# Performance work log

Hardware: AMD Instinct MI355X
Metric: run time of the kernel (lower is better)

## Reference

```python
import jax, jax.numpy as jnp
import numpy as np

NUM_EXPERT = 8
TOP_K = 2
DIM = 1024
EPS = 1e-8

def setup_inputs() -> dict:
    key = jax.random.key(0)
    ks = jax.random.split(key, 8)
    B, S, D, E, F = 2, 2048, DIM, NUM_EXPERT, 4 * DIM
    scale = 0.02
    return {
        "x": jax.random.normal(ks[0], (B, S, D), jnp.float32),
        "noise": jax.random.normal(ks[1], (B, S, E), jnp.float32),
        "gate_w": jax.random.normal(ks[2], (D, E), jnp.float32) * scale,
        "gate_b": jnp.zeros((E,), jnp.float32),
        "noise_w": jax.random.normal(ks[3], (D, E), jnp.float32) * scale,
        "noise_b": jnp.zeros((E,), jnp.float32),
        "w1": jax.random.normal(ks[4], (E, D, F), jnp.float32) * scale,
        "b1": jnp.zeros((E, F), jnp.float32),
        "w2": jax.random.normal(ks[5], (E, F, D), jnp.float32) * scale,
        "b2": jnp.zeros((E, D), jnp.float32),
    }


def reference(x, noise, gate_w, gate_b, noise_w, noise_b, w1, b1, w2, b2):
    B, S, D = x.shape
    E = gate_w.shape[-1]
    # --- router (noise passed in explicitly instead of randn_like) ---
    logits = (x @ gate_w + gate_b) + noise + (x @ noise_w + noise_b)  # [B,S,E]
    top_val, top_ids = jax.lax.top_k(logits, TOP_K)                   # [B,S,K]
    # mask of selected experts; scores = softmax over top-k logits, 0 elsewhere
    sel = jax.nn.one_hot(top_ids, E, dtype=jnp.bool_).any(axis=-2)    # [B,S,E]
    neg_inf = jnp.asarray(-jnp.inf, logits.dtype)
    scores = jax.nn.softmax(jnp.where(sel, logits, neg_inf), axis=-1)  # [B,S,E]

    flat_x = x.reshape(-1, D)            # [T,D]
    flat_s = scores.reshape(-1, E)       # [T,E]
    # dense per-expert FFN; non-selected experts have exactly-zero weight,
    # so the weighted combine matches the masked gather/scatter loop.
    h = jax.nn.silu(jnp.einsum('td,edf->etf', flat_x, w1) + b1[:, None, :])  # [E,T,F]
    eo = jnp.einsum('etf,efd->etd', h, w2) + b2[:, None, :]                  # [E,T,D]
    out = jnp.einsum('te,etd->td', flat_s, eo).reshape(B, S, D)

    # --- aux load-balancing loss: KL(uniform || importance), reduction=sum ---
    importance = flat_s.mean(axis=0)                  # [E]
    u = jnp.full_like(importance, 1.0 / E)
    aux_loss = jnp.sum(u * (jnp.log(u) - jnp.log(importance + EPS)))
    return out, aux_loss
```

## Files before the change

### kernel.cpp

```cpp
#include <hip/hip_runtime.h>
#include <hip/hip_bf16.h>
#include <cstdint>
#include <cstddef>

#define T_TOK 4096
#define D_DIM 1024
#define E_NUM 8
#define F_DIM 4096

typedef __bf16 bf16_t;
typedef bf16_t bf16x8 __attribute__((ext_vector_type(8)));
typedef float f32x4 __attribute__((ext_vector_type(4)));

__device__ __forceinline__ void gl_lds16(const void* g, void* l) {
    __builtin_amdgcn_global_load_lds(
        (const __attribute__((address_space(1))) unsigned int*)g,
        (__attribute__((address_space(3))) unsigned int*)l,
        16, 0, 0);
}

#define F_W1T    0ull
#define F_W2T    67108864ull
#define F_HT     134217728ull
#define F_XBF    209715200ull
#define F_ROWV   218103808ull
#define F_SCORES 251658240ull
#define F_TOK    (F_SCORES + 131072ull)
#define F_SC     (F_TOK    + 131072ull)
#define F_T2R    (F_SC     + 131072ull)
#define F_CNT    (F_T2R    + 32768ull)
#define F_OFF    (F_CNT    + 32ull)
#define F_BLK    (F_OFF    + 32ull)
#define FAST_NEED (F_BLK + 32ull)

#define WS_H      0ull
#define WS_ROWV   (WS_H      + 8192ull*4096*2)
#define WS_SCORES (WS_ROWV   + 8192ull*1024*4)
#define WS_TOK    (WS_SCORES + 4096ull*8*4)
#define WS_SC     (WS_TOK    + 8ull*4096*4)
#define WS_T2R    (WS_SC     + 8ull*4096*4)
#define WS_CNT    (WS_T2R    + 4096ull*2*4)
#define WS_OFF    (WS_CNT    + 32ull)
#define WS_BLK    (WS_OFF    + 32ull)

__global__ __launch_bounds__(256) void router_k(
    const float* __restrict__ x, const float* __restrict__ noise,
    const float* __restrict__ gate_w, const float* __restrict__ gate_b,
    const float* __restrict__ noise_w, const float* __restrict__ noise_b,
    float* __restrict__ scores, int* __restrict__ tok_tmp,
    float* __restrict__ sc_tmp, int* __restrict__ tok2row, int* __restrict__ counts)
{
    int t = blockIdx.x * 4 + (threadIdx.x >> 6);
    int lane = threadIdx.x & 63;
    const float* xr = x + (size_t)t * D_DIM;
    float acc[8] = {0,0,0,0,0,0,0,0};
    for (int d = lane; d < D_DIM; d += 64) {
        float xv = xr[d];
#pragma unroll
        for (int e = 0; e < 8; e++)
            acc[e] += xv * (gate_w[d*8+e] + noise_w[d*8+e]);
    }
#pragma unroll
    for (int e = 0; e < 8; e++) {
#pragma unroll
        for (int m = 1; m < 64; m <<= 1)
            acc[e] += __shfl_xor(acc[e], m);
    }
    float lg[8];
#pragma unroll
    for (int e = 0; e < 8; e++)
        lg[e] = acc[e] + gate_b[e] + noise_b[e] + noise[t*8+e];
    int e1 = 0; float v1 = lg[0];
#pragma unroll
    for (int e = 1; e < 8; e++) if (lg[e] > v1) { v1 = lg[e]; e1 = e; }
    int e2 = -1; float v2 = -INFINITY;
#pragma unroll
    for (int e = 0; e < 8; e++) if (e != e1 && lg[e] > v2) { v2 = lg[e]; e2 = e; }
    float ex = expf(v2 - v1);
    float den = 1.0f + ex;
    float s1 = 1.0f / den, s2 = ex / den;
    if (lane < 8)
        scores[t*8+lane] = (lane==e1) ? s1 : ((lane==e2) ? s2 : 0.0f);
    if (lane == 0) {
        int p1 = atomicAdd(&counts[e1], 1);
        tok_tmp[e1*T_TOK + p1] = t; sc_tmp[e1*T_TOK + p1] = s1;
        tok2row[t*2]   = (e1<<16) | p1;
        int p2 = atomicAdd(&counts[e2], 1);
        tok_tmp[e2*T_TOK + p2] = t; sc_tmp[e2*T_TOK + p2] = s2;
        tok2row[t*2+1] = (e2<<16) | p2;
    }
}

__global__ void prefix_k(const int* __restrict__ counts, int* __restrict__ offsets,
                         int* __restrict__ blk_off) {
    if (threadIdx.x == 0) {
        int o = 0, b = 0;
        for (int e = 0; e < 8; e++) {
            offsets[e] = o; blk_off[e] = b;
            o += counts[e]; b += (counts[e] + 127) >> 7;
        }
    }
}

__global__ __launch_bounds__(256) void aux_k(const float* __restrict__ scores,
                                             float* __restrict__ out_aux) {
    __shared__ float part[256];
    int i = threadIdx.x;
    int e = i & 7, g = i >> 3;
    float s = 0.f;
    for (int t = g; t < T_TOK; t += 32) s += scores[t*8+e];
    part[i] = s; __syncthreads();
    for (int st = 128; st >= 8; st >>= 1) {
        if (i < st) part[i] += part[i+st];
        __syncthreads();
    }
    if (i == 0) {
        float aux = 0.f;
        for (int ee = 0; ee < 8; ee++) {
            float imp = part[ee] * (1.0f / (float)T_TOK);
            aux += 0.125f * (logf(0.125f) - logf(imp + 1e-8f));
        }
        *out_aux = aux;
    }
}

__global__ __launch_bounds__(256) void prep_w_k(
    const float* __restrict__ src, bf16_t* __restrict__ dst,
    int ksb, int ntb, int Kdim, int Ndim)
{
    size_t cid = (size_t)blockIdx.x * 256 + threadIdx.x;
    int kc = cid & 3;
    int n  = (cid >> 2) & 127;
    int ks = (cid >> 9) & ((1 << ksb) - 1);
    int nt = (cid >> (9 + ksb)) & ((1 << ntb) - 1);
    int e  = (int)(cid >> (9 + ksb + ntb));
    int kcd = kc ^ ((n >> 1) & 3);
    int k0 = ks * 32 + kcd * 8;
    const float* s = src + ((size_t)e * Kdim + k0) * Ndim + nt * 128 + n;
    union { bf16_t u[8]; bf16x8 v; } pk;
#pragma unroll
    for (int j = 0; j < 8; j++) pk.u[j] = (bf16_t)s[(size_t)j * Ndim];
    *(bf16x8*)(dst + cid * 8) = pk.v;
}

__global__ __launch_bounds__(256) void prep_x_k(const float* __restrict__ x,
                                                bf16_t* __restrict__ xb) {
    size_t i = ((size_t)blockIdx.x * 256 + threadIdx.x) * 8;
    f32x4 a = *(const f32x4*)(x + i);
    f32x4 b = *(const f32x4*)(x + i + 4);
    union { bf16_t u[8]; bf16x8 v; } pk;
#pragma unroll
    for (int j = 0; j < 4; j++) { pk.u[j] = (bf16_t)a[j]; pk.u[4+j] = (bf16_t)b[j]; }
    *(bf16x8*)(xb + i) = pk.v;
}

__global__ __launch_bounds__(256) void ffn1_fast_k(
    const bf16_t* __restrict__ xb, const bf16_t* __restrict__ w1t,
    const float* __restrict__ b1, const int* __restrict__ tok_tmp,
    const int* __restrict__ counts, const int* __restrict__ blk_off,
    char* __restrict__ h_t)
{
    int bx = blockIdx.x;
    int nt = bx & 31, mt = (bx >> 5) & 31, e = bx >> 10;
    int ne = counts[e];
    if (mt * 128 >= ne) return;

    __shared__ alignas(16) char smem[16384];
    int tid = threadIdx.x, w = tid >> 6, l = tid & 63;

    int srow0 = w * 32 + (l >> 2);
    int kcd = (l & 3) ^ ((l >> 3) & 3);
    int g0r = mt * 128 + srow0, g1r = g0r + 16;
    int tok0 = tok_tmp[e * T_TOK + (g0r < ne ? g0r : 0)];
    int tok1 = tok_tmp[e * T_TOK + (g1r < ne ? g1r : 0)];
    const char* gA0 = (const char*)(xb + (size_t)tok0 * D_DIM + kcd * 8);
    const char* gA1 = (const char*)(xb + (size_t)tok1 * D_DIM + kcd * 8);
    const char* gB0 = (const char*)w1t + ((size_t)(e * 32 + nt) * 32) * 8192
                      + w * 2048 + l * 16;
    const char* gB1 = gB0 + 1024;
    char* lA0 = smem + w * 2048;
    char* lA1 = lA0 + 1024;
    char* lB0 = smem + 8192 + w * 2048;
    char* lB1 = lB0 + 1024;

    int fr = l & 15, kq = l >> 4;
    int csel = (kq ^ ((fr >> 1) & 3)) << 4;
    int wm = (w & 1) * 64, wn = (w >> 1) * 64;
    int aoff[4], boff[4];
#pragma unroll
    for (int i = 0; i < 4; i++) {
        aoff[i] = (wm + i * 16 + fr) * 64 + csel;
        boff[i] = 8192 + (wn + i * 16 + fr) * 64 + csel;
    }

    f32x4 acc[4][4] = {};
    for (int ks = 0; ks < 32; ks++) {
        gl_lds16(gA0, lA0); gl_lds16(gA1, lA1);
        gl_lds16(gB0, lB0); gl_lds16(gB1, lB1);
        gA0 += 64; gA1 += 64; gB0 += 8192; gB1 += 8192;
        __syncthreads();
        bf16x8 af[4], bf[4];
#pragma unroll
        for (int i = 0; i < 4; i++) af[i] = *(const bf16x8*)(smem + aoff[i]);
#pragma unroll
        for (int i = 0; i < 4; i++) bf[i] = *(const bf16x8*)(smem + boff[i]);
#pragma unroll
        for (int mi = 0; mi < 4; mi++)
#pragma unroll
            for (int ni = 0; ni < 4; ni++)
                acc[mi][ni] = __builtin_amdgcn_mfma_f32_16x16x32_bf16(af[mi], bf[ni], acc[mi][ni], 0, 0, 0);
        __syncthreads();
    }

    int quad = l >> 4;
    size_t htBase = (size_t)(blk_off[e] + mt) * 1048576ull;
    const float* b1e = b1 + (size_t)e * F_DIM + nt * 128;
    for (int rnd = 0; rnd < 4; rnd++) {
        if ((w >> 1) == (rnd >> 1)) {
            int nb0 = (rnd & 1) * 2;
#pragma unroll
            for (int nn = 0; nn < 2; nn++) {
                int cl = nn * 16 + fr;
                float bb = b1e[rnd * 32 + cl];
#pragma unroll
                for (int mi = 0; mi < 4; mi++) {
                    int rbase = wm + mi * 16 + quad * 4;
#pragma unroll
                    for (int r = 0; r < 4; r++) {
                        int row = rbase + r;
                        float v = acc[mi][nb0 + nn][r] + bb;
                        v = v / (1.0f + expf(-v));
                        int off = row * 64 + (((cl >> 3) ^ ((row >> 1) & 3)) << 4) + ((cl & 7) << 1);
                        *(bf16_t*)(smem + off) = (bf16_t)v;
                    }
                }
            }
        }
        __syncthreads();
        {
            size_t sub = htBase + (size_t)(nt * 4 + rnd) * 8192;
            *(f32x4*)(h_t + sub + tid * 16)         = *(const f32x4*)(smem + tid * 16);
            *(f32x4*)(h_t + sub + (tid + 256) * 16) = *(const f32x4*)(smem + (tid + 256) * 16);
        }
        __syncthreads();
    }
}

__global__ __launch_bounds__(256) void ffn2_fast_k(
    const char* __restrict__ h_t, const bf16_t* __restrict__ w2t,
    const float* __restrict__ b2, const float* __restrict__ sc_tmp,
    const int* __restrict__ counts, const int* __restrict__ offsets,
    const int* __restrict__ blk_off, float* __restrict__ rowv)
{
    int bx = blockIdx.x;
    int nt = bx & 7, mt = (bx >> 3) & 31, e = bx >> 8;
    int ne = counts[e];
    if (mt * 128 >= ne) return;

    __shared__ alignas(16) char smem[18944];
    int tid = threadIdx.x, w = tid >> 6, l = tid & 63;
    float* rowsc = (float*)(smem + 18432);
    if (tid < 128) {
        int r = mt * 128 + tid;
        rowsc[tid] = (r < ne) ? sc_tmp[e * T_TOK + r] : 0.0f;
    }

    const char* gA0 = h_t + (size_t)(blk_off[e] + mt) * 1048576ull + w * 2048 + l * 16;
    const char* gA1 = gA0 + 1024;
    const char* gB0 = (const char*)w2t + ((size_t)(e * 8 + nt) * 128) * 8192
                      + w * 2048 + l * 16;
    const char* gB1 = gB0 + 1024;
    char* lA0 = smem + w * 2048;
    char* lA1 = lA0 + 1024;
    char* lB0 = smem + 8192 + w * 2048;
    char* lB1 = lB0 + 1024;

    int fr = l & 15, kq = l >> 4;
    int csel = (kq ^ ((fr >> 1) & 3)) << 4;
    int wm = (w & 1) * 64, wn = (w >> 1) * 64;
    int aoff[4], boff[4];
#pragma unroll
    for (int i = 0; i < 4; i++) {
        aoff[i] = (wm + i * 16 + fr) * 64 + csel;
        boff[i] = 8192 + (wn + i * 16 + fr) * 64 + csel;
    }

    f32x4 acc[4][4] = {};
    for (int ks = 0; ks < 128; ks++) {
        gl_lds16(gA0, lA0); gl_lds16(gA1, lA1);
        gl_lds16(gB0, lB0); gl_lds16(gB1, lB1);
        gA0 += 8192; gA1 += 8192; gB0 += 8192; gB1 += 8192;
        __syncthreads();
        bf16x8 af[4], bf[4];
#pragma unroll
        for (int i = 0; i < 4; i++) af[i] = *(const bf16x8*)(smem + aoff[i]);
#pragma unroll
        for (int i = 0; i < 4; i++) bf[i] = *(const bf16x8*)(smem + boff[i]);
#pragma unroll
        for (int mi = 0; mi < 4; mi++)
#pragma unroll
            for (int ni = 0; ni < 4; ni++)
                acc[mi][ni] = __builtin_amdgcn_mfma_f32_16x16x32_bf16(af[mi], bf[ni], acc[mi][ni], 0, 0, 0);
        __syncthreads();
    }

    int quad = l >> 4;
    int off_e = offsets[e];
    const float* b2e = b2 + (size_t)e * D_DIM + nt * 128;
    float* Ct = (float*)smem;
    for (int rnd = 0; rnd < 4; rnd++) {
        if ((w >> 1) == (rnd >> 1)) {
            int nb0 = (rnd & 1) * 2;
#pragma unroll
            for (int nn = 0; nn < 2; nn++) {
                int cl = nn * 16 + fr;
                float bb = b2e[rnd * 32 + cl];
#pragma unroll
                for (int mi = 0; mi < 4; mi++) {
                    int rbase = wm + mi * 16 + quad * 4;
#pragma unroll
                    for (int r = 0; r < 4; r++) {
                        int row = rbase + r;
                        Ct[row * 36 + cl] = (acc[mi][nb0 + nn][r] + bb) * rowsc[row];
                    }
                }
            }
        }
        __syncthreads();
        {
            int row = tid >> 1, h = tid & 1;
            if (mt * 128 + row < ne) {
                float* dst = rowv + (size_t)(off_e + mt * 128 + row) * D_DIM
                           + nt * 128 + rnd * 32 + h * 16;
                const float* src = Ct + row * 36 + h * 16;
#pragma unroll
                for (int j = 0; j < 4; j++)
                    *(f32x4*)(dst + j * 4) = *(const f32x4*)(src + j * 4);
            }
        }
        __syncthreads();
    }
}

__global__ __launch_bounds__(256) void combine_k(
    const float* __restrict__ rowv, const int* __restrict__ tok2row,
    const int* __restrict__ offsets, float* __restrict__ out)
{
    int t = blockIdx.x;
    int p0 = tok2row[t*2], p1 = tok2row[t*2+1];
    int r0 = offsets[p0 >> 16] + (p0 & 0xffff);
    int r1 = offsets[p1 >> 16] + (p1 & 0xffff);
    int d = threadIdx.x * 4;
    f32x4 a = *(const f32x4*)(rowv + (size_t)r0 * D_DIM + d);
    f32x4 b = *(const f32x4*)(rowv + (size_t)r1 * D_DIM + d);
    *(f32x4*)(out + (size_t)t * D_DIM + d) = a + b;
}

#define BM 128
#define BN 128
#define BK 32
#define LDA 40
#define LDCB 136
#define LDCF 68
#define SMEM_BYTES 35328

__global__ __launch_bounds__(256) void ffn1_fb_k(
    const float* __restrict__ x, const float* __restrict__ w1, const float* __restrict__ b1,
    const int* __restrict__ tok_tmp, const int* __restrict__ counts,
    const int* __restrict__ offsets, bf16_t* __restrict__ h)
{
    int e  = blockIdx.x >> 5;
    int mt = blockIdx.x & 31;
    int nt = blockIdx.y;
    int ne = counts[e];
    if (mt * BM >= ne) return;
    int nb = nt * BN;
    const float* W = w1 + (size_t)e * D_DIM * F_DIM;

    __shared__ alignas(16) char smem[SMEM_BYTES];
    bf16_t* As = (bf16_t*)smem;
    bf16_t* Bs = (bf16_t*)(smem + 10240);
    int* rowtok = (int*)(smem + 34816);

    int tid = threadIdx.x;
    if (tid < 128) {
        int r = mt*BM + tid;
        rowtok[tid] = (r < ne) ? tok_tmp[e*T_TOK + r] : -1;
    }
    __syncthreads();

    f32x4 acc[4][4] = {};
    int wave = tid >> 6, lane = tid & 63;
    int wm = (wave & 1) * 64, wn = (wave >> 1) * 64;
    int fr = lane & 15, fk = (lane >> 4) * 8;
    int sr = tid >> 1, sh = (tid & 1) * 16;
    int bn_ = tid & 127, bk_ = (tid >> 7) * 16;

    for (int k0 = 0; k0 < D_DIM; k0 += BK) {
        {
            int tok = rowtok[sr];
            union { bf16_t u[16]; bf16x8 v[2]; } pk;
            if (tok >= 0) {
                const float* src = x + (size_t)tok * D_DIM + k0 + sh;
#pragma unroll
                for (int j = 0; j < 16; j++) pk.u[j] = (bf16_t)src[j];
            } else {
#pragma unroll
                for (int j = 0; j < 16; j++) pk.u[j] = (bf16_t)0.0f;
            }
            *(bf16x8*)(As + sr*LDA + sh)     = pk.v[0];
            *(bf16x8*)(As + sr*LDA + sh + 8) = pk.v[1];
        }
        {
            union { bf16_t u[16]; bf16x8 v[2]; } pk;
            const float* src = W + (size_t)(k0 + bk_) * F_DIM + nb + bn_;
#pragma unroll
            for (int j = 0; j < 16; j++) pk.u[j] = (bf16_t)src[(size_t)j * F_DIM];
            *(bf16x8*)(Bs + bn_*LDA + bk_)     = pk.v[0];
            *(bf16x8*)(Bs + bn_*LDA + bk_ + 8) = pk.v[1];
        }
        __syncthreads();
        bf16x8 af[4], bfr[4];
#pragma unroll
        for (int i = 0; i < 4; i++) af[i]  = *(bf16x8*)(As + (wm + i*16 + fr)*LDA + fk);
#pragma unroll
        for (int i = 0; i < 4; i++) bfr[i] = *(bf16x8*)(Bs + (wn + i*16 + fr)*LDA + fk);
#pragma unroll
        for (int mi = 0; mi < 4; mi++)
#pragma unroll
            for (int ni = 0; ni < 4; ni++)
                acc[mi][ni] = __builtin_amdgcn_mfma_f32_16x16x32_bf16(af[mi], bfr[ni], acc[mi][ni], 0, 0, 0);
        __syncthreads();
    }

    bf16_t* Ct = (bf16_t*)smem;
    const float* b1e = b1 + (size_t)e * F_DIM + nb;
#pragma unroll
    for (int mi = 0; mi < 4; mi++) {
        int row = wm + mi*16 + ((lane >> 4) << 2);
#pragma unroll
        for (int ni = 0; ni < 4; ni++) {
            int col = wn + ni*16 + fr;
            float bb = b1e[col];
#pragma unroll
            for (int r = 0; r < 4; r++) {
                float v = acc[mi][ni][r] + bb;
                float sv = v / (1.0f + expf(-v));
                Ct[(row + r)*LDCB + col] = (bf16_t)sv;
            }
        }
    }
    __syncthreads();
    {
        int row = tid >> 1, seg = (tid & 1) * 64;
        if (mt*BM + row < ne) {
            int grow = offsets[e] + mt*BM + row;
            bf16_t* dst = h + (size_t)grow * F_DIM + nb + seg;
#pragma unroll
            for (int j = 0; j < 8; j++)
                *(bf16x8*)(dst + j*8) = *(bf16x8*)(Ct + row*LDCB + seg + j*8);
        }
    }
}

__global__ __launch_bounds__(256) void ffn2_fb_k(
    const bf16_t* __restrict__ h, const float* __restrict__ w2, const float* __restrict__ b2,
    const float* __restrict__ sc_tmp, const int* __restrict__ counts,
    const int* __restrict__ offsets, float* __restrict__ rowv)
{
    int e  = blockIdx.x >> 5;
    int mt = blockIdx.x & 31;
    int nt = blockIdx.y;
    int ne = counts[e];
    if (mt * BM >= ne) return;
    int nb = nt * BN;
    int off = offsets[e];
    const float* W = w2 + (size_t)e * F_DIM * D_DIM;

    __shared__ alignas(16) char smem[SMEM_BYTES];
    bf16_t* As = (bf16_t*)smem;
    bf16_t* Bs = (bf16_t*)(smem + 10240);
    float* rowsc = (float*)(smem + 34816);

    int tid = threadIdx.x;
    if (tid < 128) {
        int r = mt*BM + tid;
        rowsc[tid] = (r < ne) ? sc_tmp[e*T_TOK + r] : 0.0f;
    }
    __syncthreads();

    f32x4 acc[4][4] = {};
    int wave = tid >> 6, lane = tid & 63;
    int wm = (wave & 1) * 64, wnn = wave >> 1;
    int fr = lane & 15, fk = (lane >> 4) * 8;
    int sr = tid >> 1, sh = (tid & 1) * 16;
    int bn_ = tid & 127, bk_ = (tid >> 7) * 16;
    bool arow_valid = (mt*BM + sr) < ne;
    const bf16_t* asrc0 = h + (size_t)(off + mt*BM + sr) * F_DIM + sh;

    for (int k0 = 0; k0 < F_DIM; k0 += BK) {
        {
            bf16x8 v0, v1;
            if (arow_valid) {
                v0 = *(const bf16x8*)(asrc0 + k0);
                v1 = *(const bf16x8*)(asrc0 + k0 + 8);
            } else {
                v0 = (bf16x8)(bf16_t)0.0f; v1 = (bf16x8)(bf16_t)0.0f;
            }
            *(bf16x8*)(As + sr*LDA + sh)     = v0;
            *(bf16x8*)(As + sr*LDA + sh + 8) = v1;
        }
        {
            union { bf16_t u[16]; bf16x8 v[2]; } pk;
            const float* src = W + (size_t)(k0 + bk_) * D_DIM + nb + bn_;
#pragma unroll
            for (int j = 0; j < 16; j++) pk.u[j] = (bf16_t)src[(size_t)j * D_DIM];
            *(bf16x8*)(Bs + bn_*LDA + bk_)     = pk.v[0];
            *(bf16x8*)(Bs + bn_*LDA + bk_ + 8) = pk.v[1];
        }
        __syncthreads();
        bf16x8 af[4], bfr[4];
#pragma unroll
        for (int i = 0; i < 4; i++) af[i]  = *(bf16x8*)(As + (wm + i*16 + fr)*LDA + fk);
#pragma unroll
        for (int i = 0; i < 4; i++) bfr[i] = *(bf16x8*)(Bs + (wnn*64 + i*16 + fr)*LDA + fk);
#pragma unroll
        for (int mi = 0; mi < 4; mi++)
#pragma unroll
            for (int ni = 0; ni < 4; ni++)
                acc[mi][ni] = __builtin_amdgcn_mfma_f32_16x16x32_bf16(af[mi], bfr[ni], acc[mi][ni], 0, 0, 0);
        __syncthreads();
    }

    const float* b2e = b2 + (size_t)e * D_DIM + nb;
    float* Ctf = (float*)smem;
    for (int half = 0; half < 2; half++) {
        if (wnn == half) {
#pragma unroll
            for (int mi = 0; mi < 4; mi++) {
                int row = wm + mi*16 + ((lane >> 4) << 2);
#pragma unroll
                for (int ni = 0; ni < 4; ni++) {
                    int lcol = ni*16 + fr;
                    float bb = b2e[half*64 + lcol];
#pragma unroll
                    for (int r = 0; r < 4; r++) {
                        float v = (acc[mi][ni][r] + bb) * rowsc[row + r];
                        Ctf[(row + r)*LDCF + lcol] = v;
                    }
                }
            }
        }
        __syncthreads();
        {
            int row = tid >> 1, seg = (tid & 1) * 32;
            if (mt*BM + row < ne) {
                float* dst = rowv + (size_t)(off + mt*BM + row) * D_DIM + nb + half*64 + seg;
#pragma unroll
                for (int j = 0; j < 8; j++)
                    *(f32x4*)(dst + j*4) = *(f32x4*)(Ctf + row*LDCF + seg + j*4);
            }
        }
        __syncthreads();
    }
}

extern "C" void kernel_launch(void* const* d_in, const int* in_sizes, int n_in,
                              void* d_out, int out_size, void* d_ws, size_t ws_size,
                              hipStream_t stream) {
    const float* x       = (const float*)d_in[0];
    const float* noise   = (const float*)d_in[1];
    const float* gate_w  = (const float*)d_in[2];
    const float* gate_b  = (const float*)d_in[3];
    const float* noise_w = (const float*)d_in[4];
    const float* noise_b = (const float*)d_in[5];
    const float* w1      = (const float*)d_in[6];
    const float* b1      = (const float*)d_in[7];
    const float* w2      = (const float*)d_in[8];
    const float* b2      = (const float*)d_in[9];
    float* out = (float*)d_out;
    char* ws = (char*)d_ws;

    if (ws_size >= FAST_NEED) {
        bf16_t* w1t     = (bf16_t*)(ws + F_W1T);
        bf16_t* w2t     = (bf16_t*)(ws + F_W2T);
        char*   h_t     = ws + F_HT;
        bf16_t* xb      = (bf16_t*)(ws + F_XBF);
        float*  rowv    = (float*) (ws + F_ROWV);
        float*  scores  = (float*) (ws + F_SCORES);
        int*    tok_tmp = (int*)   (ws + F_TOK);
        float*  sc_tmp  = (float*) (ws + F_SC);
        int*    tok2row = (int*)   (ws + F_T2R);
        int*    counts  = (int*)   (ws + F_CNT);
        int*    offsets = (int*)   (ws + F_OFF);
        int*    blk_off = (int*)   (ws + F_BLK);

        hipMemsetAsync(ws + F_CNT, 0, 32, stream);
        router_k<<<T_TOK/4, 256, 0, stream>>>(x, noise, gate_w, gate_b, noise_w, noise_b,
                                              scores, tok_tmp, sc_tmp, tok2row, counts);
        prefix_k<<<1, 64, 0, stream>>>(counts, offsets, blk_off);
        aux_k<<<1, 256, 0, stream>>>(scores, out + (size_t)T_TOK * D_DIM);
        prep_x_k<<<2048, 256, 0, stream>>>(x, xb);
        prep_w_k<<<16384, 256, 0, stream>>>(w1, w1t, 5, 5, D_DIM, F_DIM);
        prep_w_k<<<16384, 256, 0, stream>>>(w2, w2t, 7, 3, F_DIM, D_DIM);
        ffn1_fast_k<<<8192, 256, 0, stream>>>(xb, w1t, b1, tok_tmp, counts, blk_off, h_t);
        ffn2_fast_k<<<2048, 256, 0, stream>>>(h_t, w2t, b2, sc_tmp, counts, offsets, blk_off, rowv);
        combine_k<<<T_TOK, 256, 0, stream>>>(rowv, tok2row, offsets, out);
    } else {
        bf16_t* h       = (bf16_t*)(ws + WS_H);
        float*  rowv    = (float*) (ws + WS_ROWV);
        float*  scores  = (float*) (ws + WS_SCORES);
        int*    tok_tmp = (int*)   (ws + WS_TOK);
        float*  sc_tmp  = (float*) (ws + WS_SC);
        int*    tok2row = (int*)   (ws + WS_T2R);
        int*    counts  = (int*)   (ws + WS_CNT);
        int*    offsets = (int*)   (ws + WS_OFF);
        int*    blk_off = (int*)   (ws + WS_BLK);

        hipMemsetAsync(ws + WS_CNT, 0, 32, stream);
        router_k<<<T_TOK/4, 256, 0, stream>>>(x, noise, gate_w, gate_b, noise_w, noise_b,
                                              scores, tok_tmp, sc_tmp, tok2row, counts);
        prefix_k<<<1, 64, 0, stream>>>(counts, offsets, blk_off);
        aux_k<<<1, 256, 0, stream>>>(scores, out + (size_t)T_TOK * D_DIM);
        ffn1_fb_k<<<dim3(E_NUM*32, F_DIM/BN), 256, 0, stream>>>(x, w1, b1, tok_tmp, counts, offsets, h);
        ffn2_fb_k<<<dim3(E_NUM*32, D_DIM/BN), 256, 0, stream>>>(h, w2, b2, sc_tmp, counts, offsets, rowv);
        combine_k<<<T_TOK, 256, 0, stream>>>(rowv, tok2row, offsets, out);
    }
}
```

Measured before the change: 742.2 us.

## Fuse prep kernels, widen GEMM K-tiles to 64, store expert outputs as bf16

Merges the router, x conversion and both weight-transpose kernels into one launch, and the weight transpose now goes through an LDS tile so global reads are coalesced. Both FFN GEMMs double the K-step per iteration to 64, using a 32KB LDS tile with an 8-way XOR swizzle, which halves the number of barriers. The FFN1 epilogue writes the whole tile once instead of in four rounds. FFN2 writes its weighted per-row outputs as bf16, halving the traffic into the combine kernel, at some cost in precision.

```diff
diff --git a/kernel.cpp b/kernel.cpp
--- a/kernel.cpp
+++ b/kernel.cpp
@@ -10,6 +10,7 @@
 
 typedef __bf16 bf16_t;
 typedef bf16_t bf16x8 __attribute__((ext_vector_type(8)));
+typedef bf16_t bf16x4 __attribute__((ext_vector_type(4)));
 typedef float f32x4 __attribute__((ext_vector_type(4)));
 
 __device__ __forceinline__ void gl_lds16(const void* g, void* l) {
@@ -43,15 +44,14 @@
 #define WS_OFF    (WS_CNT    + 32ull)
 #define WS_BLK    (WS_OFF    + 32ull)
 
-__global__ __launch_bounds__(256) void router_k(
+__device__ __forceinline__ void router_body(
+    int t, int lane,
     const float* __restrict__ x, const float* __restrict__ noise,
     const float* __restrict__ gate_w, const float* __restrict__ gate_b,
     const float* __restrict__ noise_w, const float* __restrict__ noise_b,
     float* __restrict__ scores, int* __restrict__ tok_tmp,
     float* __restrict__ sc_tmp, int* __restrict__ tok2row, int* __restrict__ counts)
 {
-    int t = blockIdx.x * 4 + (threadIdx.x >> 6);
-    int lane = threadIdx.x & 63;
     const float* xr = x + (size_t)t * D_DIM;
     float acc[8] = {0,0,0,0,0,0,0,0};
     for (int d = lane; d < D_DIM; d += 64) {
@@ -91,13 +91,74 @@
     }
 }
 
+__global__ __launch_bounds__(256) void mega_prep_k(
+    const float* __restrict__ x, const float* __restrict__ noise,
+    const float* __restrict__ gate_w, const float* __restrict__ gate_b,
+    const float* __restrict__ noise_w, const float* __restrict__ noise_b,
+    const float* __restrict__ w1, const float* __restrict__ w2,
+    bf16_t* __restrict__ w1t, bf16_t* __restrict__ w2t, bf16_t* __restrict__ xb,
+    float* __restrict__ scores, int* __restrict__ tok_tmp,
+    float* __restrict__ sc_tmp, int* __restrict__ tok2row, int* __restrict__ counts)
+{
+    __shared__ alignas(16) float ftile[64 * 129];
+    int b = blockIdx.x, tid = threadIdx.x;
+    if (b < 8192) {
+        const float* src; bf16_t* dst; int Ndim;
+        if (b < 4096) {
+            int ks = b & 15, ntile = (b >> 4) & 31, e = b >> 9;
+            src = w1 + ((size_t)e * D_DIM + ks * 64) * F_DIM + ntile * 128;
+            Ndim = F_DIM;
+            dst = w1t + (((size_t)(e * 32 + ntile) * 16) + ks) * 8192;
+        } else {
+            int b2 = b - 4096;
+            int ks = b2 & 63, ntile = (b2 >> 6) & 7, e = b2 >> 9;
+            src = w2 + ((size_t)e * F_DIM + ks * 64) * D_DIM + ntile * 128;
+            Ndim = D_DIM;
+            dst = w2t + (((size_t)(e * 8 + ntile) * 64) + ks) * 8192;
+        }
+        int c0 = (tid & 31) * 4, r0 = tid >> 5;
+#pragma unroll
+        for (int i = 0; i < 8; i++) {
+            int r = r0 + i * 8;
+            f32x4 v = *(const f32x4*)(src + (size_t)r * Ndim + c0);
+#pragma unroll
+            for (int j = 0; j < 4; j++)
+                ftile[r * 129 + c0 + j] = v[j];
+        }
+        __syncthreads();
+#pragma unroll
+        for (int i = 0; i < 4; i++) {
+            int q = tid + i * 256;
+            int n = q >> 3, p = q & 7;
+            int c = p ^ (n & 7);
+            union { bf16_t u[8]; bf16x8 v; } pk;
+#pragma unroll
+            for (int jj = 0; jj < 8; jj++)
+                pk.u[jj] = (bf16_t)ftile[(c * 8 + jj) * 129 + n];
+            *(bf16x8*)(dst + (size_t)q * 8) = pk.v;
+        }
+    } else if (b < 10240) {
+        size_t i = ((size_t)(b - 8192) * 256 + tid) * 8;
+        f32x4 a = *(const f32x4*)(x + i);
+        f32x4 c = *(const f32x4*)(x + i + 4);
+        union { bf16_t u[8]; bf16x8 v; } pk;
+#pragma unroll
+        for (int j = 0; j < 4; j++) { pk.u[j] = (bf16_t)a[j]; pk.u[4+j] = (bf16_t)c[j]; }
+        *(bf16x8*)(xb + i) = pk.v;
+    } else {
+        int t = (b - 10240) * 4 + (tid >> 6);
+        router_body(t, tid & 63, x, noise, gate_w, gate_b, noise_w, noise_b,
+                    scores, tok_tmp, sc_tmp, tok2row, counts);
+    }
+}
+
 __global__ void prefix_k(const int* __restrict__ counts, int* __restrict__ offsets,
                          int* __restrict__ blk_off) {
     if (threadIdx.x == 0) {
-        int o = 0, b = 0;
+        int o = 0, bb = 0;
         for (int e = 0; e < 8; e++) {
-            offsets[e] = o; blk_off[e] = b;
-            o += counts[e]; b += (counts[e] + 127) >> 7;
+            offsets[e] = o; blk_off[e] = bb;
+            o += counts[e]; bb += (counts[e] + 127) >> 7;
         }
     }
 }
@@ -124,37 +185,7 @@
     }
 }
 
-__global__ __launch_bounds__(256) void prep_w_k(
-    const float* __restrict__ src, bf16_t* __restrict__ dst,
-    int ksb, int ntb, int Kdim, int Ndim)
-{
-    size_t cid = (size_t)blockIdx.x * 256 + threadIdx.x;
-    int kc = cid & 3;
-    int n  = (cid >> 2) & 127;
-    int ks = (cid >> 9) & ((1 << ksb) - 1);
-    int nt = (cid >> (9 + ksb)) & ((1 << ntb) - 1);
-    int e  = (int)(cid >> (9 + ksb + ntb));
-    int kcd = kc ^ ((n >> 1) & 3);
-    int k0 = ks * 32 + kcd * 8;
-    const float* s = src + ((size_t)e * Kdim + k0) * Ndim + nt * 128 + n;
-    union { bf16_t u[8]; bf16x8 v; } pk;
-#pragma unroll
-    for (int j = 0; j < 8; j++) pk.u[j] = (bf16_t)s[(size_t)j * Ndim];
-    *(bf16x8*)(dst + cid * 8) = pk.v;
-}
-
-__global__ __launch_bounds__(256) void prep_x_k(const float* __restrict__ x,
-                                                bf16_t* __restrict__ xb) {
-    size_t i = ((size_t)blockIdx.x * 256 + threadIdx.x) * 8;
-    f32x4 a = *(const f32x4*)(x + i);
-    f32x4 b = *(const f32x4*)(x + i + 4);
-    union { bf16_t u[8]; bf16x8 v; } pk;
-#pragma unroll
-    for (int j = 0; j < 4; j++) { pk.u[j] = (bf16_t)a[j]; pk.u[4+j] = (bf16_t)b[j]; }
-    *(bf16x8*)(xb + i) = pk.v;
-}
-
-__global__ __launch_bounds__(256) void ffn1_fast_k(
+__global__ __launch_bounds__(256) void ffn1_v3_k(
     const bf16_t* __restrict__ xb, const bf16_t* __restrict__ w1t,
     const float* __restrict__ b1, const int* __restrict__ tok_tmp,
     const int* __restrict__ counts, const int* __restrict__ blk_off,
@@ -165,184 +196,424 @@
     int ne = counts[e];
     if (mt * 128 >= ne) return;
 
-    __shared__ alignas(16) char smem[16384];
+    __shared__ alignas(16) char smem[32768];
     int tid = threadIdx.x, w = tid >> 6, l = tid & 63;
-
-    int srow0 = w * 32 + (l >> 2);
-    int kcd = (l & 3) ^ ((l >> 3) & 3);
-    int g0r = mt * 128 + srow0, g1r = g0r + 16;
-    int tok0 = tok_tmp[e * T_TOK + (g0r < ne ? g0r : 0)];
-    int tok1 = tok_tmp[e * T_TOK + (g1r < ne ? g1r : 0)];
-    const char* gA0 = (const char*)(xb + (size_t)tok0 * D_DIM + kcd * 8);
-    const char* gA1 = (const char*)(xb + (size_t)tok1 * D_DIM + kcd * 8);
-    const char* gB0 = (const char*)w1t + ((size_t)(e * 32 + nt) * 32) * 8192
-                      + w * 2048 + l * 16;
-    const char* gB1 = gB0 + 1024;
-    char* lA0 = smem + w * 2048;
-    char* lA1 = lA0 + 1024;
-    char* lB0 = smem + 8192 + w * 2048;
-    char* lB1 = lB0 + 1024;
+    int lc = (l & 7) ^ ((l >> 3) & 7);
+
+    const char* gA[4];
+#pragma unroll
+    for (int j = 0; j < 4; j++) {
+        int row = mt * 128 + w * 32 + j * 8 + (l >> 3);
+        int tok = tok_tmp[e * T_TOK + (row < ne ? row : 0)];
+        gA[j] = (const char*)xb + (size_t)tok * 2048 + lc * 16;
+    }
+    const char* gB = (const char*)w1t + (size_t)(e * 32 + nt) * 262144 + w * 4096 + l * 16;
+    char* lA = smem + w * 4096;
+    char* lB = smem + 16384 + w * 4096;
 
     int fr = l & 15, kq = l >> 4;
-    int csel = (kq ^ ((fr >> 1) & 3)) << 4;
     int wm = (w & 1) * 64, wn = (w >> 1) * 64;
-    int aoff[4], boff[4];
-#pragma unroll
-    for (int i = 0; i < 4; i++) {
-        aoff[i] = (wm + i * 16 + fr) * 64 + csel;
-        boff[i] = 8192 + (wn + i * 16 + fr) * 64 + csel;
-    }
+    int aoff[4][2], boff[4][2];
+#pragma unroll
+    for (int i = 0; i < 4; i++)
+#pragma unroll
+        for (int c2 = 0; c2 < 2; c2++) {
+            int ra = wm + i * 16 + fr;
+            aoff[i][c2] = ra * 128 + (((c2 * 4 + kq) ^ (ra & 7)) << 4);
+            int rb = wn + i * 16 + fr;
+            boff[i][c2] = 16384 + rb * 128 + (((c2 * 4 + kq) ^ (rb & 7)) << 4);
+        }
 
     f32x4 acc[4][4] = {};
-    for (int ks = 0; ks < 32; ks++) {
-        gl_lds16(gA0, lA0); gl_lds16(gA1, lA1);
-        gl_lds16(gB0, lB0); gl_lds16(gB1, lB1);
-        gA0 += 64; gA1 += 64; gB0 += 8192; gB1 += 8192;
-        __syncthreads();
-        bf16x8 af[4], bf[4];
-#pragma unroll
-        for (int i = 0; i < 4; i++) af[i] = *(const bf16x8*)(smem + aoff[i]);
-#pragma unroll
-        for (int i = 0; i < 4; i++) bf[i] = *(const bf16x8*)(smem + boff[i]);
-#pragma unroll
-        for (int mi = 0; mi < 4; mi++)
-#pragma unroll
-            for (int ni = 0; ni < 4; ni++)
-                acc[mi][ni] = __builtin_amdgcn_mfma_f32_16x16x32_bf16(af[mi], bf[ni], acc[mi][ni], 0, 0, 0);
-        __syncthreads();
-    }
-
-    int quad = l >> 4;
-    size_t htBase = (size_t)(blk_off[e] + mt) * 1048576ull;
+    for (int ks = 0; ks < 16; ks++) {
+#pragma unroll
+        for (int j = 0; j < 4; j++) {
+            gl_lds16(gA[j], lA + j * 1024);
+            gl_lds16(gB + j * 1024, lB + j * 1024);
+        }
+        gB += 16384;
+#pragma unroll
+        for (int j = 0; j < 4; j++) gA[j] += 128;
+        __syncthreads();
+        bf16x8 af[2][4], bf[2][4];
+#pragma unroll
+        for (int c2 = 0; c2 < 2; c2++)
+#pragma unroll
+            for (int i = 0; i < 4; i++) {
+                af[c2][i] = *(const bf16x8*)(smem + aoff[i][c2]);
+                bf[c2][i] = *(const bf16x8*)(smem + boff[i][c2]);
+            }
+#pragma unroll
+        for (int c2 = 0; c2 < 2; c2++)
+#pragma unroll
+            for (int mi = 0; mi < 4; mi++)
+#pragma unroll
+                for (int ni = 0; ni < 4; ni++)
+                    acc[mi][ni] = __builtin_amdgcn_mfma_f32_16x16x32_bf16(
+                        af[c2][mi], bf[c2][ni], acc[mi][ni], 0, 0, 0);
+        __syncthreads();
+    }
+
     const float* b1e = b1 + (size_t)e * F_DIM + nt * 128;
-    for (int rnd = 0; rnd < 4; rnd++) {
-        if ((w >> 1) == (rnd >> 1)) {
-            int nb0 = (rnd & 1) * 2;
-#pragma unroll
-            for (int nn = 0; nn < 2; nn++) {
-                int cl = nn * 16 + fr;
-                float bb = b1e[rnd * 32 + cl];
-#pragma unroll
-                for (int mi = 0; mi < 4; mi++) {
-                    int rbase = wm + mi * 16 + quad * 4;
-#pragma unroll
-                    for (int r = 0; r < 4; r++) {
-                        int row = rbase + r;
-                        float v = acc[mi][nb0 + nn][r] + bb;
-                        v = v / (1.0f + expf(-v));
-                        int off = row * 64 + (((cl >> 3) ^ ((row >> 1) & 3)) << 4) + ((cl & 7) << 1);
-                        *(bf16_t*)(smem + off) = (bf16_t)v;
-                    }
-                }
-            }
-        }
-        __syncthreads();
-        {
-            size_t sub = htBase + (size_t)(nt * 4 + rnd) * 8192;
-            *(f32x4*)(h_t + sub + tid * 16)         = *(const f32x4*)(smem + tid * 16);
-            *(f32x4*)(h_t + sub + (tid + 256) * 16) = *(const f32x4*)(smem + (tid + 256) * 16);
-        }
-        __syncthreads();
-    }
-}
-
-__global__ __launch_bounds__(256) void ffn2_fast_k(
+#pragma unroll
+    for (int mi = 0; mi < 4; mi++)
+#pragma unroll
+        for (int ni = 0; ni < 4; ni++) {
+            int col = wn + ni * 16 + fr;
+            float bb = b1e[col];
+#pragma unroll
+            for (int r = 0; r < 4; r++) {
+                int row = wm + mi * 16 + kq * 4 + r;
+                float v = acc[mi][ni][r] + bb;
+                v = v / (1.0f + expf(-v));
+                int off = (col >> 6) * 16384 + row * 128
+                        + ((((col & 63) >> 3) ^ (row & 7)) << 4) + ((col & 7) << 1);
+                *(bf16_t*)(smem + off) = (bf16_t)v;
+            }
+        }
+    __syncthreads();
+    {
+        char* dst = h_t + (size_t)(blk_off[e] + mt) * 1048576ull
+                  + (size_t)nt * 32768 + tid * 16;
+        const char* src = smem + tid * 16;
+#pragma unroll
+        for (int i = 0; i < 8; i++)
+            *(f32x4*)(dst + i * 4096) = *(const f32x4*)(src + i * 4096);
+    }
+}
+
+__global__ __launch_bounds__(256) void ffn2_v3_k(
     const char* __restrict__ h_t, const bf16_t* __restrict__ w2t,
     const float* __restrict__ b2, const float* __restrict__ sc_tmp,
     const int* __restrict__ counts, const int* __restrict__ offsets,
-    const int* __restrict__ blk_off, float* __restrict__ rowv)
+    const int* __restrict__ blk_off, bf16_t* __restrict__ rowv)
 {
     int bx = blockIdx.x;
     int nt = bx & 7, mt = (bx >> 3) & 31, e = bx >> 8;
     int ne = counts[e];
     if (mt * 128 >= ne) return;
 
-    __shared__ alignas(16) char smem[18944];
+    __shared__ alignas(16) char smem[35328];
+    float* rowsc = (float*)(smem + 34816);
     int tid = threadIdx.x, w = tid >> 6, l = tid & 63;
-    float* rowsc = (float*)(smem + 18432);
     if (tid < 128) {
         int r = mt * 128 + tid;
         rowsc[tid] = (r < ne) ? sc_tmp[e * T_TOK + r] : 0.0f;
     }
 
-    const char* gA0 = h_t + (size_t)(blk_off[e] + mt) * 1048576ull + w * 2048 + l * 16;
-    const char* gA1 = gA0 + 1024;
-    const char* gB0 = (const char*)w2t + ((size_t)(e * 8 + nt) * 128) * 8192
-                      + w * 2048 + l * 16;
-    const char* gB1 = gB0 + 1024;
-    char* lA0 = smem + w * 2048;
-    char* lA1 = lA0 + 1024;
-    char* lB0 = smem + 8192 + w * 2048;
-    char* lB1 = lB0 + 1024;
+    const char* gA = h_t + (size_t)(blk_off[e] + mt) * 1048576ull + w * 4096 + l * 16;
+    const char* gB = (const char*)w2t + (size_t)(e * 8 + nt) * 1048576ull + w * 4096 + l * 16;
+    char* lA = smem + w * 4096;
+    char* lB = smem + 16384 + w * 4096;
 
     int fr = l & 15, kq = l >> 4;
-    int csel = (kq ^ ((fr >> 1) & 3)) << 4;
     int wm = (w & 1) * 64, wn = (w >> 1) * 64;
-    int aoff[4], boff[4];
-#pragma unroll
-    for (int i = 0; i < 4; i++) {
-        aoff[i] = (wm + i * 16 + fr) * 64 + csel;
-        boff[i] = 8192 + (wn + i * 16 + fr) * 64 + csel;
-    }
+    int aoff[4][2], boff[4][2];
+#pragma unroll
+    for (int i = 0; i < 4; i++)
+#pragma unroll
+        for (int c2 = 0; c2 < 2; c2++) {
+            int ra = wm + i * 16 + fr;
+            aoff[i][c2] = ra * 128 + (((c2 * 4 + kq) ^ (ra & 7)) << 4);
+            int rb = wn + i * 16 + fr;
+            boff[i][c2] = 16384 + rb * 128 + (((c2 * 4 + kq) ^ (rb & 7)) << 4);
+        }
 
     f32x4 acc[4][4] = {};
-    for (int ks = 0; ks < 128; ks++) {
-        gl_lds16(gA0, lA0); gl_lds16(gA1, lA1);
-        gl_lds16(gB0, lB0); gl_lds16(gB1, lB1);
-        gA0 += 8192; gA1 += 8192; gB0 += 8192; gB1 += 8192;
-        __syncthreads();
-        bf16x8 af[4], bf[4];
-#pragma unroll
-        for (int i = 0; i < 4; i++) af[i] = *(const bf16x8*)(smem + aoff[i]);
-#pragma unroll
-        for (int i = 0; i < 4; i++) bf[i] = *(const bf16x8*)(smem + boff[i]);
+    for (int ks = 0; ks < 64; ks++) {
+#pragma unroll
+        for (int j = 0; j < 4; j++) {
+            gl_lds16(gA + j * 1024, lA + j * 1024);
+            gl_lds16(gB + j * 1024, lB + j * 1024);
+        }
+        gA += 16384; gB += 16384;
+        __syncthreads();
+        bf16x8 af[2][4], bf[2][4];
+#pragma unroll
+        for (int c2 = 0; c2 < 2; c2++)
+#pragma unroll
+            for (int i = 0; i < 4; i++) {
+                af[c2][i] = *(const bf16x8*)(smem + aoff[i][c2]);
+                bf[c2][i] = *(const bf16x8*)(smem + boff[i][c2]);
+            }
+#pragma unroll
+        for (int c2 = 0; c2 < 2; c2++)
+#pragma unroll
+            for (int mi = 0; mi < 4; mi++)
+#pragma unroll
+                for (int ni = 0; ni < 4; ni++)
+                    acc[mi][ni] = __builtin_amdgcn_mfma_f32_16x16x32_bf16(
+                        af[c2][mi], bf[c2][ni], acc[mi][ni], 0, 0, 0);
+        __syncthreads();
+    }
+
+    const float* b2e = b2 + (size_t)e * D_DIM + nt * 128;
+#pragma unroll
+    for (int mi = 0; mi < 4; mi++)
+#pragma unroll
+        for (int ni = 0; ni < 4; ni++) {
+            int col = wn + ni * 16 + fr;
+            float bb = b2e[col];
+#pragma unroll
+            for (int r = 0; r < 4; r++) {
+                int row = wm + mi * 16 + kq * 4 + r;
+                float v = (acc[mi][ni][r] + bb) * rowsc[row];
+                *(bf16_t*)(smem + row * 272 + col * 2) = (bf16_t)v;
+            }
+        }
+    __syncthreads();
+    {
+        int row = tid >> 1, half = tid & 1;
+        if (mt * 128 + row < ne) {
+            char* dst = (char*)rowv + (size_t)(offsets[e] + mt * 128 + row) * 2048
+                      + nt * 256 + half * 128;
+            const char* src = smem + row * 272 + half * 128;
+#pragma unroll
+            for (int j = 0; j < 8; j++)
+                *(f32x4*)(dst + j * 16) = *(const f32x4*)(src + j * 16);
+        }
+    }
+}
+
+__global__ __launch_bounds__(256) void combine_v3_k(
+    const bf16_t* __restrict__ rowv, const int* __restrict__ tok2row,
+    const int* __restrict__ offsets, float* __restrict__ out)
+{
+    int t = blockIdx.x;
+    int p0 = tok2row[t*2], p1 = tok2row[t*2+1];
+    int r0 = offsets[p0 >> 16] + (p0 & 0xffff);
+    int r1 = offsets[p1 >> 16] + (p1 & 0xffff);
+    int d = threadIdx.x * 4;
+    bf16x4 a = *(const bf16x4*)(rowv + (size_t)r0 * D_DIM + d);
+    bf16x4 b = *(const bf16x4*)(rowv + (size_t)r1 * D_DIM + d);
+    f32x4 o;
+#pragma unroll
+    for (int j = 0; j < 4; j++) o[j] = (float)a[j] + (float)b[j];
+    *(f32x4*)(out + (size_t)t * D_DIM + d) = o;
+}
+
+#define BM 128
+#define BN 128
+#define BK 32
+#define LDA 40
+#define LDCB 136
+#define LDCF 68
+#define SMEM_BYTES 35328
+
+__global__ __launch_bounds__(256) void router_fb_k(
+    const float* __restrict__ x, const float* __restrict__ noise,
+    const float* __restrict__ gate_w, const float* __restrict__ gate_b,
+    const float* __restrict__ noise_w, const float* __restrict__ noise_b,
+    float* __restrict__ scores, int* __restrict__ tok_tmp,
+    float* __restrict__ sc_tmp, int* __restrict__ tok2row, int* __restrict__ counts)
+{
+    int t = blockIdx.x * 4 + (threadIdx.x >> 6);
+    router_body(t, threadIdx.x & 63, x, noise, gate_w, gate_b, noise_w, noise_b,
+                scores, tok_tmp, sc_tmp, tok2row, counts);
+}
+
+__global__ __launch_bounds__(256) void ffn1_fb_k(
+    const float* __restrict__ x, const float* __restrict__ w1, const float* __restrict__ b1,
+    const int* __restrict__ tok_tmp, const int* __restrict__ counts,
+    const int* __restrict__ offsets, bf16_t* __restrict__ h)
+{
+    int e  = blockIdx.x >> 5;
+    int mt = blockIdx.x & 31;
+    int nt = blockIdx.y;
+    int ne = counts[e];
+    if (mt * BM >= ne) return;
+    int nb = nt * BN;
+    const float* W = w1 + (size_t)e * D_DIM * F_DIM;
+
+    __shared__ alignas(16) char smem[SMEM_BYTES];
+    bf16_t* As = (bf16_t*)smem;
+    bf16_t* Bs = (bf16_t*)(smem + 10240);
+    int* rowtok = (int*)(smem + 34816);
+
+    int tid = threadIdx.x;
+    if (tid < 128) {
+        int r = mt*BM + tid;
+        rowtok[tid] = (r < ne) ? tok_tmp[e*T_TOK + r] : -1;
+    }
+    __syncthreads();
+
+    f32x4 acc[4][4] = {};
+    int wave = tid >> 6, lane = tid & 63;
+    int wm = (wave & 1) * 64, wn = (wave >> 1) * 64;
+    int fr = lane & 15, fk = (lane >> 4) * 8;
+    int sr = tid >> 1, sh = (tid & 1) * 16;
+    int bn_ = tid & 127, bk_ = (tid >> 7) * 16;
+
+    for (int k0 = 0; k0 < D_DIM; k0 += BK) {
+        {
+            int tok = rowtok[sr];
+            union { bf16_t u[16]; bf16x8 v[2]; } pk;
+            if (tok >= 0) {
+                const float* src = x + (size_t)tok * D_DIM + k0 + sh;
+#pragma unroll
+                for (int j = 0; j < 16; j++) pk.u[j] = (bf16_t)src[j];
+            } else {
+#pragma unroll
+                for (int j = 0; j < 16; j++) pk.u[j] = (bf16_t)0.0f;
+            }
+            *(bf16x8*)(As + sr*LDA + sh)     = pk.v[0];
+            *(bf16x8*)(As + sr*LDA + sh + 8) = pk.v[1];
+        }
+        {
+            union { bf16_t u[16]; bf16x8 v[2]; } pk;
+            const float* src = W + (size_t)(k0 + bk_) * F_DIM + nb + bn_;
+#pragma unroll
+            for (int j = 0; j < 16; j++) pk.u[j] = (bf16_t)src[(size_t)j * F_DIM];
+            *(bf16x8*)(Bs + bn_*LDA + bk_)     = pk.v[0];
+            *(bf16x8*)(Bs + bn_*LDA + bk_ + 8) = pk.v[1];
+        }
+        __syncthreads();
+        bf16x8 af[4], bfr[4];
+#pragma unroll
+        for (int i = 0; i < 4; i++) af[i]  = *(bf16x8*)(As + (wm + i*16 + fr)*LDA + fk);
+#pragma unroll
+        for (int i = 0; i < 4; i++) bfr[i] = *(bf16x8*)(Bs + (wn + i*16 + fr)*LDA + fk);
 #pragma unroll
         for (int mi = 0; mi < 4; mi++)
 #pragma unroll
             for (int ni = 0; ni < 4; ni++)
-                acc[mi][ni] = __builtin_amdgcn_mfma_f32_16x16x32_bf16(af[mi], bf[ni], acc[mi][ni], 0, 0, 0);
-        __syncthreads();
-    }
-
-    int quad = l >> 4;
-    int off_e = offsets[e];
-    const float* b2e = b2 + (size_t)e * D_DIM + nt * 128;
-    float* Ct = (float*)smem;
-    for (int rnd = 0; rnd < 4; rnd++) {
-        if ((w >> 1) == (rnd >> 1)) {
-            int nb0 = (rnd & 1) * 2;
-#pragma unroll
-            for (int nn = 0; nn < 2; nn++) {
-                int cl = nn * 16 + fr;
-                float bb = b2e[rnd * 32 + cl];
-#pragma unroll
-                for (int mi = 0; mi < 4; mi++) {
-                    int rbase = wm + mi * 16 + quad * 4;
+                acc[mi][ni] = __builtin_amdgcn_mfma_f32_16x16x32_bf16(af[mi], bfr[ni], acc[mi][ni], 0, 0, 0);
+        __syncthreads();
+    }
+
+    bf16_t* Ct = (bf16_t*)smem;
+    const float* b1e = b1 + (size_t)e * F_DIM + nb;
+#pragma unroll
+    for (int mi = 0; mi < 4; mi++) {
+        int row = wm + mi*16 + ((lane >> 4) << 2);
+#pragma unroll
+        for (int ni = 0; ni < 4; ni++) {
+            int col = wn + ni*16 + fr;
+            float bb = b1e[col];
+#pragma unroll
+            for (int r = 0; r < 4; r++) {
+                float v = acc[mi][ni][r] + bb;
+                float sv = v / (1.0f + expf(-v));
+                Ct[(row + r)*LDCB + col] = (bf16_t)sv;
+            }
+        }
+    }
+    __syncthreads();
+    {
+        int row = tid >> 1, seg = (tid & 1) * 64;
+        if (mt*BM + row < ne) {
+            int grow = offsets[e] + mt*BM + row;
+            bf16_t* dst = h + (size_t)grow * F_DIM + nb + seg;
+#pragma unroll
+            for (int j = 0; j < 8; j++)
+                *(bf16x8*)(dst + j*8) = *(bf16x8*)(Ct + row*LDCB + seg + j*8);
+        }
+    }
+}
+
+__global__ __launch_bounds__(256) void ffn2_fb_k(
+    const bf16_t* __restrict__ h, const float* __restrict__ w2, const float* __restrict__ b2,
+    const float* __restrict__ sc_tmp, const int* __restrict__ counts,
+    const int* __restrict__ offsets, float* __restrict__ rowv)
+{
+    int e  = blockIdx.x >> 5;
+    int mt = blockIdx.x & 31;
+    int nt = blockIdx.y;
+    int ne = counts[e];
+    if (mt * BM >= ne) return;
+    int nb = nt * BN;
+    int off = offsets[e];
+    const float* W = w2 + (size_t)e * F_DIM * D_DIM;
+
+    __shared__ alignas(16) char smem[SMEM_BYTES];
+    bf16_t* As = (bf16_t*)smem;
+    bf16_t* Bs = (bf16_t*)(smem + 10240);
+    float* rowsc = (float*)(smem + 34816);
+
+    int tid = threadIdx.x;
+    if (tid < 128) {
+        int r = mt*BM + tid;
+        rowsc[tid] = (r < ne) ? sc_tmp[e*T_TOK + r] : 0.0f;
+    }
+    __syncthreads();
+
+    f32x4 acc[4][4] = {};
+    int wave = tid >> 6, lane = tid & 63;
+    int wm = (wave & 1) * 64, wnn = wave >> 1;
+    int fr = lane & 15, fk = (lane >> 4) * 8;
+    int sr = tid >> 1, sh = (tid & 1) * 16;
+    int bn_ = tid & 127, bk_ = (tid >> 7) * 16;
+    bool arow_valid = (mt*BM + sr) < ne;
+    const bf16_t* asrc0 = h + (size_t)(off + mt*BM + sr) * F_DIM + sh;
+
+    for (int k0 = 0; k0 < F_DIM; k0 += BK) {
+        {
+            bf16x8 v0, v1;
+            if (arow_valid) {
+                v0 = *(const bf16x8*)(asrc0 + k0);
+                v1 = *(const bf16x8*)(asrc0 + k0 + 8);
+            } else {
+                v0 = (bf16x8)(bf16_t)0.0f; v1 = (bf16x8)(bf16_t)0.0f;
+            }
+            *(bf16x8*)(As + sr*LDA + sh)     = v0;
+            *(bf16x8*)(As + sr*LDA + sh + 8) = v1;
+        }
+        {
+            union { bf16_t u[16]; bf16x8 v[2]; } pk;
+            const float* src = W + (size_t)(k0 + bk_) * D_DIM + nb + bn_;
+#pragma unroll
+            for (int j = 0; j < 16; j++) pk.u[j] = (bf16_t)src[(size_t)j * D_DIM];
+            *(bf16x8*)(Bs + bn_*LDA + bk_)     = pk.v[0];
+            *(bf16x8*)(Bs + bn_*LDA + bk_ + 8) = pk.v[1];
+        }
+        __syncthreads();
+        bf16x8 af[4], bfr[4];
+#pragma unroll
+        for (int i = 0; i < 4; i++) af[i]  = *(bf16x8*)(As + (wm + i*16 + fr)*LDA + fk);
+#pragma unroll
+        for (int i = 0; i < 4; i++) bfr[i] = *(bf16x8*)(Bs + (wnn*64 + i*16 + fr)*LDA + fk);
+#pragma unroll
+        for (int mi = 0; mi < 4; mi++)
+#pragma unroll
+            for (int ni = 0; ni < 4; ni++)
+                acc[mi][ni] = __builtin_amdgcn_mfma_f32_16x16x32_bf16(af[mi], bfr[ni], acc[mi][ni], 0, 0, 0);
+        __syncthreads();
+    }
+
+    const float* b2e = b2 + (size_t)e * D_DIM + nb;
+    float* Ctf = (float*)smem;
+    for (int half = 0; half < 2; half++) {
+        if (wnn == half) {
+#pragma unroll
+            for (int mi = 0; mi < 4; mi++) {
+                int row = wm + mi*16 + ((lane >> 4) << 2);
+#pragma unroll
+                for (int ni = 0; ni < 4; ni++) {
+                    int lcol = ni*16 + fr;
+                    float bb = b2e[half*64 + lcol];
 #pragma unroll
                     for (int r = 0; r < 4; r++) {
-                        int row = rbase + r;
-                        Ct[row * 36 + cl] = (acc[mi][nb0 + nn][r] + bb) * rowsc[row];
+                        float v = (acc[mi][ni][r] + bb) * rowsc[row + r];
+                        Ctf[(row + r)*LDCF + lcol] = v;
                     }
                 }
             }
         }
         __syncthreads();
         {
-            int row = tid >> 1, h = tid & 1;
-            if (mt * 128 + row < ne) {
-                float* dst = rowv + (size_t)(off_e + mt * 128 + row) * D_DIM
-                           + nt * 128 + rnd * 32 + h * 16;
-                const float* src = Ct + row * 36 + h * 16;
-#pragma unroll
-                for (int j = 0; j < 4; j++)
-                    *(f32x4*)(dst + j * 4) = *(const f32x4*)(src + j * 4);
-            }
-        }
-        __syncthreads();
-    }
-}
-
-__global__ __launch_bounds__(256) void combine_k(
+            int row = tid >> 1, seg = (tid & 1) * 32;
+            if (mt*BM + row < ne) {
+                float* dst = rowv + (size_t)(off + mt*BM + row) * D_DIM + nb + half*64 + seg;
+#pragma unroll
+                for (int j = 0; j < 8; j++)
+                    *(f32x4*)(dst + j*4) = *(f32x4*)(Ctf + row*LDCF + seg + j*4);
+            }
+        }
+        __syncthreads();
+    }
+}
+
+__global__ __launch_bounds__(256) void combine_fb_k(
     const float* __restrict__ rowv, const int* __restrict__ tok2row,
     const int* __restrict__ offsets, float* __restrict__ out)
 {
@@ -354,215 +625,6 @@
     f32x4 a = *(const f32x4*)(rowv + (size_t)r0 * D_DIM + d);
     f32x4 b = *(const f32x4*)(rowv + (size_t)r1 * D_DIM + d);
     *(f32x4*)(out + (size_t)t * D_DIM + d) = a + b;
-}
-
-#define BM 128
-#define BN 128
-#define BK 32
-#define LDA 40
-#define LDCB 136
-#define LDCF 68
-#define SMEM_BYTES 35328
-
-__global__ __launch_bounds__(256) void ffn1_fb_k(
-    const float* __restrict__ x, const float* __restrict__ w1, const float* __restrict__ b1,
-    const int* __restrict__ tok_tmp, const int* __restrict__ counts,
-    const int* __restrict__ offsets, bf16_t* __restrict__ h)
-{
-    int e  = blockIdx.x >> 5;
-    int mt = blockIdx.x & 31;
-    int nt = blockIdx.y;
-    int ne = counts[e];
-    if (mt * BM >= ne) return;
-    int nb = nt * BN;
-    const float* W = w1 + (size_t)e * D_DIM * F_DIM;
-
-    __shared__ alignas(16) char smem[SMEM_BYTES];
-    bf16_t* As = (bf16_t*)smem;
-    bf16_t* Bs = (bf16_t*)(smem + 10240);
-    int* rowtok = (int*)(smem + 34816);
-
-    int tid = threadIdx.x;
-    if (tid < 128) {
-        int r = mt*BM + tid;
-        rowtok[tid] = (r < ne) ? tok_tmp[e*T_TOK + r] : -1;
-    }
-    __syncthreads();
-
-    f32x4 acc[4][4] = {};
-    int wave = tid >> 6, lane = tid & 63;
-    int wm = (wave & 1) * 64, wn = (wave >> 1) * 64;
-    int fr = lane & 15, fk = (lane >> 4) * 8;
-    int sr = tid >> 1, sh = (tid & 1) * 16;
-    int bn_ = tid & 127, bk_ = (tid >> 7) * 16;
-
-    for (int k0 = 0; k0 < D_DIM; k0 += BK) {
-        {
-            int tok = rowtok[sr];
-            union { bf16_t u[16]; bf16x8 v[2]; } pk;
-            if (tok >= 0) {
-                const float* src = x + (size_t)tok * D_DIM + k0 + sh;
-#pragma unroll
-                for (int j = 0; j < 16; j++) pk.u[j] = (bf16_t)src[j];
-            } else {
-#pragma unroll
-                for (int j = 0; j < 16; j++) pk.u[j] = (bf16_t)0.0f;
-            }
-            *(bf16x8*)(As + sr*LDA + sh)     = pk.v[0];
-            *(bf16x8*)(As + sr*LDA + sh + 8) = pk.v[1];
-        }
-        {
-            union { bf16_t u[16]; bf16x8 v[2]; } pk;
-            const float* src = W + (size_t)(k0 + bk_) * F_DIM + nb + bn_;
-#pragma unroll
-            for (int j = 0; j < 16; j++) pk.u[j] = (bf16_t)src[(size_t)j * F_DIM];
-            *(bf16x8*)(Bs + bn_*LDA + bk_)     = pk.v[0];
-            *(bf16x8*)(Bs + bn_*LDA + bk_ + 8) = pk.v[1];
-        }
-        __syncthreads();
-        bf16x8 af[4], bfr[4];
-#pragma unroll
-        for (int i = 0; i < 4; i++) af[i]  = *(bf16x8*)(As + (wm + i*16 + fr)*LDA + fk);
-#pragma unroll
-        for (int i = 0; i < 4; i++) bfr[i] = *(bf16x8*)(Bs + (wn + i*16 + fr)*LDA + fk);
-#pragma unroll
-        for (int mi = 0; mi < 4; mi++)
-#pragma unroll
-            for (int ni = 0; ni < 4; ni++)
-                acc[mi][ni] = __builtin_amdgcn_mfma_f32_16x16x32_bf16(af[mi], bfr[ni], acc[mi][ni], 0, 0, 0);
-        __syncthreads();
-    }
-
-    bf16_t* Ct = (bf16_t*)smem;
-    const float* b1e = b1 + (size_t)e * F_DIM + nb;
-#pragma unroll
-    for (int mi = 0; mi < 4; mi++) {
-        int row = wm + mi*16 + ((lane >> 4) << 2);
-#pragma unroll
-        for (int ni = 0; ni < 4; ni++) {
-            int col = wn + ni*16 + fr;
-            float bb = b1e[col];
-#pragma unroll
-            for (int r = 0; r < 4; r++) {
-                float v = acc[mi][ni][r] + bb;
-                float sv = v / (1.0f + expf(-v));
-                Ct[(row + r)*LDCB + col] = (bf16_t)sv;
-            }
-        }
-    }
-    __syncthreads();
-    {
-        int row = tid >> 1, seg = (tid & 1) * 64;
-        if (mt*BM + row < ne) {
-            int grow = offsets[e] + mt*BM + row;
-            bf16_t* dst = h + (size_t)grow * F_DIM + nb + seg;
-#pragma unroll
-            for (int j = 0; j < 8; j++)
-                *(bf16x8*)(dst + j*8) = *(bf16x8*)(Ct + row*LDCB + seg + j*8);
-        }
-    }
-}
-
-__global__ __launch_bounds__(256) void ffn2_fb_k(
-    const bf16_t* __restrict__ h, const float* __restrict__ w2, const float* __restrict__ b2,
-    const float* __restrict__ sc_tmp, const int* __restrict__ counts,
-    const int* __restrict__ offsets, float* __restrict__ rowv)
-{
-    int e  = blockIdx.x >> 5;
-    int mt = blockIdx.x & 31;
-    int nt = blockIdx.y;
-    int ne = counts[e];
-    if (mt * BM >= ne) return;
-    int nb = nt * BN;
-    int off = offsets[e];
-    const float* W = w2 + (size_t)e * F_DIM * D_DIM;
-
-    __shared__ alignas(16) char smem[SMEM_BYTES];
-    bf16_t* As = (bf16_t*)smem;
-    bf16_t* Bs = (bf16_t*)(smem + 10240);
-    float* rowsc = (float*)(smem + 34816);
-
-    int tid = threadIdx.x;
-    if (tid < 128) {
-        int r = mt*BM + tid;
-        rowsc[tid] = (r < ne) ? sc_tmp[e*T_TOK + r] : 0.0f;
-    }
-    __syncthreads();
-
-    f32x4 acc[4][4] = {};
-    int wave = tid >> 6, lane = tid & 63;
-    int wm = (wave & 1) * 64, wnn = wave >> 1;
-    int fr = lane & 15, fk = (lane >> 4) * 8;
-    int sr = tid >> 1, sh = (tid & 1) * 16;
-    int bn_ = tid & 127, bk_ = (tid >> 7) * 16;
-    bool arow_valid = (mt*BM + sr) < ne;
-    const bf16_t* asrc0 = h + (size_t)(off + mt*BM + sr) * F_DIM + sh;
-
-    for (int k0 = 0; k0 < F_DIM; k0 += BK) {
-        {
-            bf16x8 v0, v1;
-            if (arow_valid) {
-                v0 = *(const bf16x8*)(asrc0 + k0);
-                v1 = *(const bf16x8*)(asrc0 + k0 + 8);
-            } else {
-                v0 = (bf16x8)(bf16_t)0.0f; v1 = (bf16x8)(bf16_t)0.0f;
-            }
-            *(bf16x8*)(As + sr*LDA + sh)     = v0;
-            *(bf16x8*)(As + sr*LDA + sh + 8) = v1;
-        }
-        {
-            union { bf16_t u[16]; bf16x8 v[2]; } pk;
-            const float* src = W + (size_t)(k0 + bk_) * D_DIM + nb + bn_;
-#pragma unroll
-            for (int j = 0; j < 16; j++) pk.u[j] = (bf16_t)src[(size_t)j * D_DIM];
-            *(bf16x8*)(Bs + bn_*LDA + bk_)     = pk.v[0];
-            *(bf16x8*)(Bs + bn_*LDA + bk_ + 8) = pk.v[1];
-        }
-        __syncthreads();
-        bf16x8 af[4], bfr[4];
-#pragma unroll
-        for (int i = 0; i < 4; i++) af[i]  = *(bf16x8*)(As + (wm + i*16 + fr)*LDA + fk);
-#pragma unroll
-        for (int i = 0; i < 4; i++) bfr[i] = *(bf16x8*)(Bs + (wnn*64 + i*16 + fr)*LDA + fk);
-#pragma unroll
-        for (int mi = 0; mi < 4; mi++)
-#pragma unroll
-            for (int ni = 0; ni < 4; ni++)
-                acc[mi][ni] = __builtin_amdgcn_mfma_f32_16x16x32_bf16(af[mi], bfr[ni], acc[mi][ni], 0, 0, 0);
-        __syncthreads();
-    }
-
-    const float* b2e = b2 + (size_t)e * D_DIM + nb;
-    float* Ctf = (float*)smem;
-    for (int half = 0; half < 2; half++) {
-        if (wnn == half) {
-#pragma unroll
-            for (int mi = 0; mi < 4; mi++) {
-                int row = wm + mi*16 + ((lane >> 4) << 2);
-#pragma unroll
-                for (int ni = 0; ni < 4; ni++) {
-                    int lcol = ni*16 + fr;
-                    float bb = b2e[half*64 + lcol];
-#pragma unroll
-                    for (int r = 0; r < 4; r++) {
-                        float v = (acc[mi][ni][r] + bb) * rowsc[row + r];
-                        Ctf[(row + r)*LDCF + lcol] = v;
-                    }
-                }
-            }
-        }
-        __syncthreads();
-        {
-            int row = tid >> 1, seg = (tid & 1) * 32;
-            if (mt*BM + row < ne) {
-                float* dst = rowv + (size_t)(off + mt*BM + row) * D_DIM + nb + half*64 + seg;
-#pragma unroll
-                for (int j = 0; j < 8; j++)
-                    *(f32x4*)(dst + j*4) = *(f32x4*)(Ctf + row*LDCF + seg + j*4);
-            }
-        }
-        __syncthreads();
-    }
 }
 
 extern "C" void kernel_launch(void* const* d_in, const int* in_sizes, int n_in,
@@ -586,7 +648,7 @@
         bf16_t* w2t     = (bf16_t*)(ws + F_W2T);
         char*   h_t     = ws + F_HT;
         bf16_t* xb      = (bf16_t*)(ws + F_XBF);
-        float*  rowv    = (float*) (ws + F_ROWV);
+        bf16_t* rowv    = (bf16_t*)(ws + F_ROWV);
         float*  scores  = (float*) (ws + F_SCORES);
         int*    tok_tmp = (int*)   (ws + F_TOK);
         float*  sc_tmp  = (float*) (ws + F_SC);
@@ -596,16 +658,14 @@
         int*    blk_off = (int*)   (ws + F_BLK);
 
         hipMemsetAsync(ws + F_CNT, 0, 32, stream);
-        router_k<<<T_TOK/4, 256, 0, stream>>>(x, noise, gate_w, gate_b, noise_w, noise_b,
-                                              scores, tok_tmp, sc_tmp, tok2row, counts);
+        mega_prep_k<<<11264, 256, 0, stream>>>(x, noise, gate_w, gate_b, noise_w, noise_b,
+                                               w1, w2, w1t, w2t, xb,
+                                               scores, tok_tmp, sc_tmp, tok2row, counts);
         prefix_k<<<1, 64, 0, stream>>>(counts, offsets, blk_off);
         aux_k<<<1, 256, 0, stream>>>(scores, out + (size_t)T_TOK * D_DIM);
-        prep_x_k<<<2048, 256, 0, stream>>>(x, xb);
-        prep_w_k<<<16384, 256, 0, stream>>>(w1, w1t, 5, 5, D_DIM, F_DIM);
-        prep_w_k<<<16384, 256, 0, stream>>>(w2, w2t, 7, 3, F_DIM, D_DIM);
-        ffn1_fast_k<<<8192, 256, 0, stream>>>(xb, w1t, b1, tok_tmp, counts, blk_off, h_t);
-        ffn2_fast_k<<<2048, 256, 0, stream>>>(h_t, w2t, b2, sc_tmp, counts, offsets, blk_off, rowv);
-        combine_k<<<T_TOK, 256, 0, stream>>>(rowv, tok2row, offsets, out);
+        ffn1_v3_k<<<8192, 256, 0, stream>>>(xb, w1t, b1, tok_tmp, counts, blk_off, h_t);
+        ffn2_v3_k<<<2048, 256, 0, stream>>>(h_t, w2t, b2, sc_tmp, counts, offsets, blk_off, rowv);
+        combine_v3_k<<<T_TOK, 256, 0, stream>>>(rowv, tok2row, offsets, out);
     } else {
         bf16_t* h       = (bf16_t*)(ws + WS_H);
         float*  rowv    = (float*) (ws + WS_ROWV);
@@ -615,15 +675,14 @@
         int*    tok2row = (int*)   (ws + WS_T2R);
         int*    counts  = (int*)   (ws + WS_CNT);
         int*    offsets = (int*)   (ws + WS_OFF);
-        int*    blk_off = (int*)   (ws + WS_BLK);
 
         hipMemsetAsync(ws + WS_CNT, 0, 32, stream);
-        router_k<<<T_TOK/4, 256, 0, stream>>>(x, noise, gate_w, gate_b, noise_w, noise_b,
-                                              scores, tok_tmp, sc_tmp, tok2row, counts);
-        prefix_k<<<1, 64, 0, stream>>>(counts, offsets, blk_off);
+        router_fb_k<<<T_TOK/4, 256, 0, stream>>>(x, noise, gate_w, gate_b, noise_w, noise_b,
+                                                 scores, tok_tmp, sc_tmp, tok2row, counts);
+        prefix_k<<<1, 64, 0, stream>>>(counts, offsets, (int*)(ws + WS_BLK));
         aux_k<<<1, 256, 0, stream>>>(scores, out + (size_t)T_TOK * D_DIM);
         ffn1_fb_k<<<dim3(E_NUM*32, F_DIM/BN), 256, 0, stream>>>(x, w1, b1, tok_tmp, counts, offsets, h);
         ffn2_fb_k<<<dim3(E_NUM*32, D_DIM/BN), 256, 0, stream>>>(h, w2, b2, sc_tmp, counts, offsets, rowv);
-        combine_k<<<T_TOK, 256, 0, stream>>>(rowv, tok2row, offsets, out);
-    }
-}
+        combine_fb_k<<<T_TOK, 256, 0, stream>>>(rowv, tok2row, offsets, out);
+    }
+}
```

Result: no change. 745.0 us (+0.4%).
